# Kernel optimization log

Measured on AMD Instinct MI355X. Metric: run time of the kernel, lower is better.

Reference implementation:

```python
import jax, jax.numpy as jnp
import numpy as np

# RosaAttention config constants
H = 16       # num_rosa_heads
KV = 4       # num_rosa_key_value_heads
QKB = 64     # num_rosa_query_key_bits
VB = 64      # num_rosa_value_bits
HID = 2048   # hidden_size
TAU = 1.0    # temperature buffer


def setup_inputs() -> dict:
    key = jax.random.key(0)
    ks = jax.random.split(key, 8)
    B, S = 2, 2048
    sc = 0.02
    return {
        "x": jax.random.normal(ks[0], (B, S, HID), jnp.float32),
        "attention_mask": jnp.ones((B, S), jnp.int32),
        "Wq": jax.random.normal(ks[1], (HID, H * QKB), jnp.float32) * sc,
        "Wk": jax.random.normal(ks[2], (HID, KV * QKB), jnp.float32) * sc,
        "Wv": jax.random.normal(ks[3], (HID, KV * VB), jnp.float32) * sc,
        "Wo": jax.random.normal(ks[4], (H * VB, HID), jnp.float32) * sc,
        "emb0": jnp.full((H, VB), -1e-05, jnp.float32),
        "emb1": jnp.full((H, VB), +1e-05, jnp.float32),
    }


def reference(x, attention_mask, Wq, Wk, Wv, Wo, emb0, emb1):
    B, S, _ = x.shape
    rep = H // KV
    # projections -> [b, s, heads, bits]
    xq = (x @ Wq).reshape(B, S, H, QKB)
    xk = (x @ Wk).reshape(B, S, KV, QKB)
    xv = (x @ Wv).reshape(B, S, KV, VB)
    # repeat_kv: each kv head repeated n_rep times contiguously
    xk = jnp.repeat(xk, rep, axis=2)   # [b, s, H, QKB]
    xv = jnp.repeat(xv, rep, axis=2)   # [b, s, H, VB]
    # soft bit quantization of q/k, tau-scaled bit-similarity score
    qb = jnp.tanh(xq)
    kb = jnp.tanh(xk)
    scores = jnp.einsum('bqhd,bkhd->bhqk', qb, kb) / (TAU * QKB)
    # causal mask + padding mask (mask True = attend)
    causal = jnp.tril(jnp.ones((S, S), bool))
    mask = causal[None, None] & attention_mask.astype(bool)[:, None, None, :]
    scores = jnp.where(mask, scores, jnp.finfo(scores.dtype).min)
    probs = jax.nn.softmax(scores, axis=-1)        # [b, h, q, k]
    # soft-binarized values: per-bit probabilities, attended, then mapped
    # through learned per-head bit embeddings emb0 (bit=0) / emb1 (bit=1)
    vp = jax.nn.sigmoid(xv)                        # [b, s, H, VB]
    ctx = jnp.einsum('bhqk,bkhv->bqhv', probs, vp) # [b, s, H, VB]
    out_bits = ctx * emb1[None, None] + (1.0 - ctx) * emb0[None, None]
    out = out_bits.reshape(B, S, H * VB) @ Wo      # [b, s, HID]
    return out
```

## Files before the change

kernel.cpp:

```cpp
#include <hip/hip_runtime.h>
#include <math.h>

typedef short bf16x8 __attribute__((ext_vector_type(8)));
typedef float f32x4 __attribute__((ext_vector_type(4)));
typedef float f32x16 __attribute__((ext_vector_type(16)));
typedef unsigned int u32x2 __attribute__((ext_vector_type(2)));
typedef unsigned int u32x4 __attribute__((ext_vector_type(4)));

#define MFMA_BF16(A,B,C) __builtin_amdgcn_mfma_f32_16x16x32_bf16(A,B,C,0,0,0)
#define MFMA32(A,B,C)    __builtin_amdgcn_mfma_f32_32x32x16_bf16(A,B,C,0,0,0)

#define VMCNT(N) asm volatile("s_waitcnt vmcnt(" #N ")" ::: "memory")
#define RBAR() do { asm volatile("" ::: "memory"); __builtin_amdgcn_s_barrier(); \
                    asm volatile("" ::: "memory"); } while (0)
#define PERMSWAP(a, b) asm volatile("v_permlane32_swap_b32 %0, %1" : "+v"(a), "+v"(b))

__device__ __forceinline__ unsigned short f2b(float x) {
    union { float f; unsigned int u; } v; v.f = x;
    unsigned int r = v.u + 0x7FFFu + ((v.u >> 16) & 1u);
    return (unsigned short)(r >> 16);
}

__device__ __forceinline__ unsigned int cvtpk(float lo, float hi) {
    unsigned int r;
    asm("v_cvt_pk_bf16_f32 %0, %1, %2" : "=v"(r) : "v"(lo), "v"(hi));
    return r;
}

__device__ __forceinline__ void gload16(const unsigned short* g, unsigned short* l) {
    __builtin_amdgcn_global_load_lds(
        (const __attribute__((address_space(1))) unsigned int*)(g),
        (__attribute__((address_space(3))) unsigned int*)(l),
        16, 0, 0);
}

__global__ __launch_bounds__(256) void conv_bf16(const float* __restrict__ s,
                                                 unsigned short* __restrict__ d, int n)
{
    int i = blockIdx.x * blockDim.x + threadIdx.x;
    int stride = gridDim.x * blockDim.x;
    for (int idx = i * 4; idx < n; idx += stride * 4) {
        float4 v = *(const float4*)(s + idx);
        ushort4 o;
        o.x = f2b(v.x); o.y = f2b(v.y); o.z = f2b(v.z); o.w = f2b(v.w);
        *(ushort4*)(d + idx) = o;
    }
}

__global__ __launch_bounds__(256) void transp_conv_qkv(const float* __restrict__ Wq,
                                                       const float* __restrict__ Wk,
                                                       const float* __restrict__ Wv,
                                                       unsigned short* __restrict__ dst)
{
    __shared__ float t[32][33];
    const int tx = threadIdx.x, ty = threadIdx.y;
    int bx = blockIdx.x;
    const float* src; int C, cb, dco;
    if (bx < 32)      { src = Wq; C = 1024; cb = bx;      dco = 0; }
    else if (bx < 40) { src = Wk; C = 256;  cb = bx - 32; dco = 1024; }
    else              { src = Wv; C = 256;  cb = bx - 40; dco = 1280; }
    const int c = cb * 32 + tx;
    const int r0 = blockIdx.y * 32;
#pragma unroll
    for (int i = 0; i < 4; ++i)
        t[ty + i * 8][tx] = src[(size_t)(r0 + ty + i * 8) * C + c];
    __syncthreads();
    const int cc = cb * 32 + ty;
#pragma unroll
    for (int i = 0; i < 4; ++i)
        dst[(size_t)(dco + cc + i * 8) * 2048 + r0 + tx] = f2b(t[tx][ty + i * 8]);
}

__global__ __launch_bounds__(256) void transp_conv(const float* __restrict__ src, int R, int C,
                                                   unsigned short* __restrict__ dst, int pitch)
{
    __shared__ float t[32][33];
    const int tx = threadIdx.x, ty = threadIdx.y;
    const int c = blockIdx.x * 32 + tx;
    const int r0 = blockIdx.y * 32;
#pragma unroll
    for (int i = 0; i < 4; ++i)
        t[ty + i * 8][tx] = src[(size_t)(r0 + ty + i * 8) * C + c];
    __syncthreads();
    const int cc = blockIdx.x * 32 + ty;
#pragma unroll
    for (int i = 0; i < 4; ++i)
        dst[(size_t)(cc + i * 8) * pitch + r0 + tx] = f2b(t[tx][ty + i * 8]);
}

__device__ __forceinline__ void stage_g(const unsigned short* AgL, const unsigned short* BgL,
                                        int K, int k0s,
                                        unsigned short* Asb, unsigned short* Bsb, int w)
{
#pragma unroll
    for (int t = 0; t < 4; ++t) {
        const int sub = t >> 1, half = t & 1;
        gload16(AgL + (size_t)(half * 16) * K + k0s + sub * 32,
                Asb + sub * 4096 + (w * 2 + half) * 512);
    }
#pragma unroll
    for (int kk = 0; kk < 2; ++kk)
        gload16(BgL + k0s + kk * 32, Bsb + kk * 2048 + w * 512);
}

template <int MODE>
__global__ __launch_bounds__(256, 3) void gemm_bt_mfma(
    const unsigned short* __restrict__ A,
    const unsigned short* __restrict__ Bt,
    int M, int N, int K,
    float* __restrict__ Cf,
    unsigned short* __restrict__ qh,
    unsigned short* __restrict__ kh,
    unsigned short* __restrict__ vtt)
{
    __shared__ __align__(16) unsigned short As[2][2 * 128 * 32];
    __shared__ __align__(16) unsigned short Bs[2][2 * 64 * 32];

    const int tid = threadIdx.x;
    const int w = tid >> 6, lane = tid & 63, l15 = lane & 15, quad = lane >> 4;
    const int wm = w & 1, wn = w >> 1;
    const int m0 = blockIdx.y * 128, n0 = blockIdx.x * 64;

    const int dsrow = lane >> 2;
    const int dscol = ((lane & 3) ^ ((lane >> 3) & 3)) * 8;
    const int sl8   = (((lane & 15) << 2) | ((lane >> 4) ^ ((lane >> 1) & 3))) * 8;

    f32x4 acc[4][2];
    const f32x4 zero4 = {0.f, 0.f, 0.f, 0.f};
#pragma unroll
    for (int i = 0; i < 4; ++i)
#pragma unroll
        for (int j = 0; j < 2; ++j) acc[i][j] = zero4;

    const unsigned short* AgL = A  + (size_t)(m0 + w * 32 + dsrow) * K + dscol;
    const unsigned short* BgL = Bt + (size_t)(n0 + w * 16 + dsrow) * K + dscol;

    const int NT = K >> 6;
    stage_g(AgL, BgL, K, 0, &As[0][0], &Bs[0][0], w);

    int cb = 0;
    for (int t = 0; t < NT; ++t) {
        if (t + 1 < NT) {
            stage_g(AgL, BgL, K, (t + 1) * 64, &As[cb ^ 1][0], &Bs[cb ^ 1][0], w);
            VMCNT(6);
        } else {
            VMCNT(0);
        }
        RBAR();

        bf16x8 af[4][2], bf[2][2];
#pragma unroll
        for (int kk = 0; kk < 2; ++kk) {
#pragma unroll
            for (int mt = 0; mt < 4; ++mt)
                af[mt][kk] = *(const bf16x8*)&As[cb][kk * 4096 + (wm * 4 + mt) * 512 + sl8];
#pragma unroll
            for (int nt = 0; nt < 2; ++nt)
                bf[nt][kk] = *(const bf16x8*)&Bs[cb][kk * 2048 + (wn * 2 + nt) * 512 + sl8];
        }
#pragma unroll
        for (int kk = 0; kk < 2; ++kk)
#pragma unroll
            for (int mt = 0; mt < 4; ++mt)
#pragma unroll
                for (int nt = 0; nt < 2; ++nt)
                    acc[mt][nt] = MFMA_BF16(af[mt][kk], bf[nt][kk], acc[mt][nt]);

        if (t + 1 < NT) RBAR();
        cb ^= 1;
    }

    if (MODE == 0) {
#pragma unroll
        for (int mt = 0; mt < 4; ++mt)
#pragma unroll
            for (int nt = 0; nt < 2; ++nt) {
                const int gn = n0 + wn * 32 + nt * 16 + l15;
#pragma unroll
                for (int r = 0; r < 4; ++r) {
                    const int gm = m0 + wm * 64 + mt * 16 + quad * 4 + r;
                    Cf[(size_t)gm * N + gn] = acc[mt][nt][r];
                }
            }
    } else {
        if (n0 < 1024) {
#pragma unroll
            for (int mt = 0; mt < 4; ++mt)
#pragma unroll
                for (int nt = 0; nt < 2; ++nt) {
                    const int gn = n0 + wn * 32 + nt * 16 + l15;
#pragma unroll
                    for (int r = 0; r < 4; ++r) {
                        const int gm = m0 + wm * 64 + mt * 16 + quad * 4 + r;
                        qh[(size_t)gm * 1024 + gn] = f2b(tanhf(acc[mt][nt][r]) * 0.0225421100f);
                    }
                }
        } else if (n0 < 1280) {
#pragma unroll
            for (int mt = 0; mt < 4; ++mt)
#pragma unroll
                for (int nt = 0; nt < 2; ++nt) {
                    const int gn = n0 + wn * 32 + nt * 16 + l15 - 1024;
#pragma unroll
                    for (int r = 0; r < 4; ++r) {
                        const int gm = m0 + wm * 64 + mt * 16 + quad * 4 + r;
                        kh[(size_t)gm * 256 + gn] = f2b(tanhf(acc[mt][nt][r]));
                    }
                }
        } else {
#pragma unroll
            for (int mt = 0; mt < 4; ++mt)
#pragma unroll
                for (int nt = 0; nt < 2; ++nt) {
                    const int gn = n0 + wn * 32 + nt * 16 + l15 - 1280;
                    const int g = gn >> 6, vv = gn & 63;
                    const int s0 = m0 + wm * 64 + mt * 16 + quad * 4;
                    const int b = s0 >> 11, sl = s0 & 2047;
                    ushort4 pk;
                    unsigned short* pp = (unsigned short*)&pk;
#pragma unroll
                    for (int r = 0; r < 4; ++r) {
                        float sv = 1.0f / (1.0f + __expf(-acc[mt][nt][r]));
                        pp[r] = f2b(sv);
                    }
                    *(ushort4*)&vtt[((size_t)(b * 4 + g) * 64 + vv) * 2048 + sl] = pk;
                }
        }
    }
}

__global__ __launch_bounds__(256, 4) void rosa_attn_mfma(
    const unsigned short* __restrict__ qh,
    const unsigned short* __restrict__ kh,
    const unsigned short* __restrict__ vtt,
    const int* __restrict__ amask,
    const float* __restrict__ emb0,
    const float* __restrict__ emb1,
    unsigned short* __restrict__ ob)
{
    __shared__ __align__(16) unsigned short Ks[2][4096];
    __shared__ __align__(16) unsigned short Vs[2][4096];
    __shared__ unsigned int Mflg[4];
    __shared__ float Lred[2][2][32];

    const int a = blockIdx.x & 7, m = blockIdx.x >> 3;
    const int h = blockIdx.y, b = blockIdx.z, g = h >> 2;
    const int hb = h + 16 * b;
    const int sel = (m + (hb >> 3)) & 3;
    const int qt = (sel == 0) ? a : (sel == 1) ? 15 - a : (sel == 2) ? 16 + a : 31 - a;

    const int tid = threadIdx.x;
    const int w = tid >> 6, lane = tid & 63;
    const int kq = w >> 1, qq = w & 1;
    const int l31 = lane & 31, H = lane >> 5, x7 = lane & 7;

    const int srow = lane >> 3;
    const int scol = ((lane & 7) ^ srow) * 8;
    const unsigned short* kst0 = kh + ((size_t)(b * 2048) + w * 16 + srow) * 256 + g * 64 + scol;
    const unsigned short* vst0 = vtt + ((size_t)(b * 4 + g) * 64 + w * 16 + srow) * 2048 + scol;
    const int* mbase = amask + b * 2048;

    int kadr[4];
#pragma unroll
    for (int mi = 0; mi < 4; ++mi)
        kadr[mi] = (kq * 32 + l31) * 64 + (((mi * 2 + H) ^ x7) * 8);
    int vadr[2][2];
#pragma unroll
    for (int vh = 0; vh < 2; ++vh)
#pragma unroll
        for (int kc = 0; kc < 2; ++kc)
            vadr[vh][kc] = (vh * 32 + l31) * 64 + (((kq * 4 + kc * 2 + H) ^ x7) * 8);

    unsigned int cbits = 0;
#pragma unroll
    for (int r = 0; r < 16; ++r) {
        const int kl = (r & 3) + 8 * (r >> 2) + 4 * H;
        if (kl <= l31) cbits |= (1u << r);
    }

    const int q0 = qt * 64, nkt = qt + 1;

#define STAGE_TILE(k0s, buf)                                                   \
    {                                                                          \
        gload16(kst0 + (size_t)(k0s) * 256,        &Ks[buf][(w * 16) * 64]);   \
        gload16(kst0 + (size_t)(k0s) * 256 + 2048, &Ks[buf][(w * 16 + 8) * 64]);\
        gload16(vst0 + (k0s),                      &Vs[buf][(w * 16) * 64]);   \
        gload16(vst0 + (k0s) + 16384,              &Vs[buf][(w * 16 + 8) * 64]);\
    }

    const int4 mv0 = *(const int4*)(mbase + tid * 8);
    const int4 mv1 = *(const int4*)(mbase + tid * 8 + 4);

    STAGE_TILE(0, 0)

    const unsigned short* qp = qh + ((size_t)(b * 2048 + q0 + qq * 32 + l31) * 16 + h) * 64 + H * 8;
    const bf16x8 qf0 = *(const bf16x8*)(qp);
    const bf16x8 qf1 = *(const bf16x8*)(qp + 16);
    const bf16x8 qf2 = *(const bf16x8*)(qp + 32);
    const bf16x8 qf3 = *(const bf16x8*)(qp + 48);

    const bool f8 = mv0.x && mv0.y && mv0.z && mv0.w && mv1.x && mv1.y && mv1.z && mv1.w;
    const unsigned long long bal = __ballot(f8);
    const bool bytefull = ((bal >> ((lane & 7) * 8)) & 0xFFull) == 0xFFull;
    const unsigned long long bal2 = __ballot(bytefull && (lane < 8));
    if (lane == 0) Mflg[w] = (unsigned int)(bal2 & 0xFFull);
    RBAR();
    const unsigned int mflags = Mflg[0] | (Mflg[1] << 8) | (Mflg[2] << 16) | (Mflg[3] << 24);

    const f32x16 z16 = {0.f,0.f,0.f,0.f, 0.f,0.f,0.f,0.f, 0.f,0.f,0.f,0.f, 0.f,0.f,0.f,0.f};
    f32x16 oacc0 = z16, oacc1 = z16;
    float psum = 0.0f;
    const bool skipdiag = (kq > qq);

    int cb = 0;
    for (int kt = 0; kt < nkt; ++kt) {
        if (kt + 1 < nkt) {
            STAGE_TILE((kt + 1) * 64, cb ^ 1)
            VMCNT(4);
        } else {
            VMCNT(0);
        }
        RBAR();

        const bool diag = (kt == qt);
        if (!(diag && skipdiag)) {
            const bf16x8 kf0 = *(const bf16x8*)&Ks[cb][kadr[0]];
            const bf16x8 kf1 = *(const bf16x8*)&Ks[cb][kadr[1]];
            const bf16x8 kf2 = *(const bf16x8*)&Ks[cb][kadr[2]];
            const bf16x8 kf3 = *(const bf16x8*)&Ks[cb][kadr[3]];
            __builtin_amdgcn_s_setprio(1);
            f32x16 sc = MFMA32(kf0, qf0, z16);
            sc = MFMA32(kf1, qf1, sc);
            sc = MFMA32(kf2, qf2, sc);
            sc = MFMA32(kf3, qf3, sc);
            __builtin_amdgcn_s_setprio(0);

            float p[16];
#pragma unroll
            for (int r = 0; r < 16; ++r) p[r] = __builtin_exp2f(sc[r]);
            if (diag && kq == qq) {
#pragma unroll
                for (int r = 0; r < 16; ++r)
                    if (!((cbits >> r) & 1u)) p[r] = 0.0f;
            }
            if (!((mflags >> kt) & 1u)) {
#pragma unroll
                for (int r = 0; r < 16; ++r) {
                    const int kgl = kt * 64 + kq * 32 + (r & 3) + 8 * (r >> 2) + 4 * H;
                    if (mbase[kgl] == 0) p[r] = 0.0f;
                }
            }
            psum += (((p[0]+p[1])+(p[2]+p[3])) + ((p[4]+p[5])+(p[6]+p[7])))
                  + (((p[8]+p[9])+(p[10]+p[11])) + ((p[12]+p[13])+(p[14]+p[15])));

            unsigned int W0 = cvtpk(p[0],  p[1]),  W1 = cvtpk(p[2],  p[3]);
            unsigned int W2 = cvtpk(p[4],  p[5]),  W3 = cvtpk(p[6],  p[7]);
            unsigned int W4 = cvtpk(p[8],  p[9]),  W5 = cvtpk(p[10], p[11]);
            unsigned int W6 = cvtpk(p[12], p[13]), W7 = cvtpk(p[14], p[15]);
            PERMSWAP(W0, W2);  PERMSWAP(W1, W3);
            PERMSWAP(W4, W6);  PERMSWAP(W5, W7);
            u32x4 paw0; paw0[0] = W0; paw0[1] = W1; paw0[2] = W2; paw0[3] = W3;
            u32x4 paw1; paw1[0] = W4; paw1[1] = W5; paw1[2] = W6; paw1[3] = W7;
            const bf16x8 pa0 = __builtin_bit_cast(bf16x8, paw0);
            const bf16x8 pa1 = __builtin_bit_cast(bf16x8, paw1);

            const bf16x8 vb00 = *(const bf16x8*)&Vs[cb][vadr[0][0]];
            const bf16x8 vb01 = *(const bf16x8*)&Vs[cb][vadr[0][1]];
            const bf16x8 vb10 = *(const bf16x8*)&Vs[cb][vadr[1][0]];
            const bf16x8 vb11 = *(const bf16x8*)&Vs[cb][vadr[1][1]];
            __builtin_amdgcn_s_setprio(1);
            oacc0 = MFMA32(pa0, vb00, oacc0);
            oacc0 = MFMA32(pa1, vb01, oacc0);
            oacc1 = MFMA32(pa0, vb10, oacc1);
            oacc1 = MFMA32(pa1, vb11, oacc1);
            __builtin_amdgcn_s_setprio(0);
        }

        if (kt + 1 < nkt) { RBAR(); cb ^= 1; }
    }

    psum += __shfl_xor(psum, 32);

    RBAR();

    if (H == 0) Lred[kq][qq][l31] = psum;

    float* Ored = (float*)&Ks[0][0];
    const int slw = qq * 2 + (1 - kq);
    if (kq == 0) {
#pragma unroll
        for (int c = 0; c < 4; ++c) {
            float4 t = {oacc1[c*4+0], oacc1[c*4+1], oacc1[c*4+2], oacc1[c*4+3]};
            *(float4*)&Ored[slw * 1024 + lane * 16 + ((c ^ (lane & 3)) * 4)] = t;
        }
    } else {
#pragma unroll
        for (int c = 0; c < 4; ++c) {
            float4 t = {oacc0[c*4+0], oacc0[c*4+1], oacc0[c*4+2], oacc0[c*4+3]};
            *(float4*)&Ored[slw * 1024 + lane * 16 + ((c ^ (lane & 3)) * 4)] = t;
        }
    }
    RBAR();

    const int slr = qq * 2 + kq;
    f32x16 osum = (kq == 0) ? oacc0 : oacc1;
#pragma unroll
    for (int c = 0; c < 4; ++c) {
        float4 t = *(const float4*)&Ored[slr * 1024 + lane * 16 + ((c ^ (lane & 3)) * 4)];
        osum[c*4+0] += t.x; osum[c*4+1] += t.y; osum[c*4+2] += t.z; osum[c*4+3] += t.w;
    }

    float rl[16];
#pragma unroll
    for (int r = 0; r < 16; ++r) {
        const int ql = (r & 3) + 8 * (r >> 2) + 4 * H;
        rl[r] = __builtin_amdgcn_rcpf(Lred[0][qq][ql] + Lred[1][qq][ql]);
    }

    const int vg = kq * 32 + l31;
    const float e0 = emb0[h * 64 + vg];
    const float ed = emb1[h * 64 + vg] - e0;
    unsigned short* obp = ob + ((size_t)(b * 2048 + q0 + qq * 32) * 16 + h) * 64 + vg;
#pragma unroll
    for (int r = 0; r < 16; ++r) {
        const int ql = (r & 3) + 8 * (r >> 2) + 4 * H;
        const float val = e0 + (osum[r] * rl[r]) * ed;
        obp[(size_t)ql * 1024] = f2b(val);
    }
#undef STAGE_TILE
}

extern "C" void kernel_launch(void* const* d_in, const int* in_sizes, int n_in,
                              void* d_out, int out_size, void* d_ws, size_t ws_size,
                              hipStream_t stream)
{
    const float* x    = (const float*)d_in[0];
    const int*   amask= (const int*)d_in[1];
    const float* Wq   = (const float*)d_in[2];
    const float* Wk   = (const float*)d_in[3];
    const float* Wv   = (const float*)d_in[4];
    const float* Wo   = (const float*)d_in[5];
    const float* emb0 = (const float*)d_in[6];
    const float* emb1 = (const float*)d_in[7];
    float* out = (float*)d_out;

    char* base = (char*)d_ws;
    unsigned short* xh    = (unsigned short*)(base);
    unsigned short* ob    = xh;
    unsigned short* Wqkvt = (unsigned short*)(base + (16u << 20));
    unsigned short* Wot   = (unsigned short*)(base + (22u << 20));
    unsigned short* qh    = (unsigned short*)(base + (26u << 20));
    unsigned short* kh    = (unsigned short*)(base + (34u << 20));
    unsigned short* vtt   = (unsigned short*)(base + (36u << 20));

    conv_bf16<<<2048, 256, 0, stream>>>(x, xh, 4096 * 2048);
    transp_conv_qkv<<<dim3(48, 64), dim3(32, 8), 0, stream>>>(Wq, Wk, Wv, Wqkvt);
    transp_conv<<<dim3(64, 32), dim3(32, 8), 0, stream>>>(Wo, 1024, 2048, Wot, 1024);

    gemm_bt_mfma<1><<<dim3(24, 32), 256, 0, stream>>>(xh, Wqkvt, 4096, 1536, 2048,
                                                      nullptr, qh, kh, vtt);
    rosa_attn_mfma<<<dim3(32, 16, 2), 256, 0, stream>>>(qh, kh, vtt, amask, emb0, emb1, ob);
    gemm_bt_mfma<0><<<dim3(32, 32), 256, 0, stream>>>(ob, Wot, 4096, 2048, 1024,
                                                      out, nullptr, nullptr, nullptr);
}
```

Before: 223.6 us.

## Fuse prep kernels, remap GEMM block order, enlarge output GEMM tile, reswizzle LDS

Merges the three conversion/transpose kernels into one prep launch to remove launch overhead and tail gaps. Splits the templated GEMM into a dedicated QKV kernel and an output-projection kernel. The output GEMM now uses 128x128 tiles with a larger LDS footprint and occupancy 2. Both GEMMs get a blockIdx remap that groups tiles for L2 locality. The attention reduction scratch gets a different XOR swizzle meant to cut LDS bank conflicts.

```diff
diff --git a/kernel.cpp b/kernel.cpp
--- a/kernel.cpp
+++ b/kernel.cpp
@@ -34,63 +34,69 @@
         16, 0, 0);
 }
 
-__global__ __launch_bounds__(256) void conv_bf16(const float* __restrict__ s,
-                                                 unsigned short* __restrict__ d, int n)
-{
-    int i = blockIdx.x * blockDim.x + threadIdx.x;
-    int stride = gridDim.x * blockDim.x;
-    for (int idx = i * 4; idx < n; idx += stride * 4) {
-        float4 v = *(const float4*)(s + idx);
-        ushort4 o;
-        o.x = f2b(v.x); o.y = f2b(v.y); o.z = f2b(v.z); o.w = f2b(v.w);
-        *(ushort4*)(d + idx) = o;
-    }
-}
-
-__global__ __launch_bounds__(256) void transp_conv_qkv(const float* __restrict__ Wq,
-                                                       const float* __restrict__ Wk,
-                                                       const float* __restrict__ Wv,
-                                                       unsigned short* __restrict__ dst)
+__global__ __launch_bounds__(256) void prep(
+    const float* __restrict__ x, unsigned short* __restrict__ xh,
+    const float* __restrict__ Wq, const float* __restrict__ Wk,
+    const float* __restrict__ Wv, unsigned short* __restrict__ Wqkvt,
+    const float* __restrict__ Wo, unsigned short* __restrict__ Wot)
 {
     __shared__ float t[32][33];
-    const int tx = threadIdx.x, ty = threadIdx.y;
-    int bx = blockIdx.x;
-    const float* src; int C, cb, dco;
-    if (bx < 32)      { src = Wq; C = 1024; cb = bx;      dco = 0; }
-    else if (bx < 40) { src = Wk; C = 256;  cb = bx - 32; dco = 1024; }
-    else              { src = Wv; C = 256;  cb = bx - 40; dco = 1280; }
-    const int c = cb * 32 + tx;
-    const int r0 = blockIdx.y * 32;
-#pragma unroll
-    for (int i = 0; i < 4; ++i)
-        t[ty + i * 8][tx] = src[(size_t)(r0 + ty + i * 8) * C + c];
-    __syncthreads();
-    const int cc = cb * 32 + ty;
-#pragma unroll
-    for (int i = 0; i < 4; ++i)
-        dst[(size_t)(dco + cc + i * 8) * 2048 + r0 + tx] = f2b(t[tx][ty + i * 8]);
-}
-
-__global__ __launch_bounds__(256) void transp_conv(const float* __restrict__ src, int R, int C,
-                                                   unsigned short* __restrict__ dst, int pitch)
-{
-    __shared__ float t[32][33];
-    const int tx = threadIdx.x, ty = threadIdx.y;
-    const int c = blockIdx.x * 32 + tx;
-    const int r0 = blockIdx.y * 32;
-#pragma unroll
-    for (int i = 0; i < 4; ++i)
-        t[ty + i * 8][tx] = src[(size_t)(r0 + ty + i * 8) * C + c];
-    __syncthreads();
-    const int cc = blockIdx.x * 32 + ty;
-#pragma unroll
-    for (int i = 0; i < 4; ++i)
-        dst[(size_t)(cc + i * 8) * pitch + r0 + tx] = f2b(t[tx][ty + i * 8]);
-}
-
-__device__ __forceinline__ void stage_g(const unsigned short* AgL, const unsigned short* BgL,
-                                        int K, int k0s,
-                                        unsigned short* Asb, unsigned short* Bsb, int w)
+    const int bid = blockIdx.x, tid = threadIdx.x;
+
+    if (bid < 2048) {
+        const int n = 4096 * 2048;
+        int i = bid * 256 + tid;
+        int stride = 2048 * 256;
+        for (int idx = i * 4; idx < n; idx += stride * 4) {
+            float4 v = *(const float4*)(x + idx);
+            ushort4 o;
+            o.x = f2b(v.x); o.y = f2b(v.y); o.z = f2b(v.z); o.w = f2b(v.w);
+            *(ushort4*)(xh + idx) = o;
+        }
+        return;
+    }
+
+    const int tx = tid & 31, ty = tid >> 5;
+
+    if (bid < 5120) {
+        const int idx = bid - 2048;
+        const int bx = idx % 48, by = idx / 48;
+        const float* src; int C, cb, dco;
+        if (bx < 32)      { src = Wq; C = 1024; cb = bx;      dco = 0; }
+        else if (bx < 40) { src = Wk; C = 256;  cb = bx - 32; dco = 1024; }
+        else              { src = Wv; C = 256;  cb = bx - 40; dco = 1280; }
+        const int c = cb * 32 + tx;
+        const int r0 = by * 32;
+#pragma unroll
+        for (int i = 0; i < 4; ++i)
+            t[ty + i * 8][tx] = src[(size_t)(r0 + ty + i * 8) * C + c];
+        __syncthreads();
+        const int cc = cb * 32 + ty;
+#pragma unroll
+        for (int i = 0; i < 4; ++i)
+            Wqkvt[(size_t)(dco + cc + i * 8) * 2048 + r0 + tx] = f2b(t[tx][ty + i * 8]);
+        return;
+    }
+
+    {
+        const int idx = bid - 5120;
+        const int bx = idx % 64, by = idx / 64;
+        const int c = bx * 32 + tx;
+        const int r0 = by * 32;
+#pragma unroll
+        for (int i = 0; i < 4; ++i)
+            t[ty + i * 8][tx] = Wo[(size_t)(r0 + ty + i * 8) * 2048 + c];
+        __syncthreads();
+        const int cc = bx * 32 + ty;
+#pragma unroll
+        for (int i = 0; i < 4; ++i)
+            Wot[(size_t)(cc + i * 8) * 1024 + r0 + tx] = f2b(t[tx][ty + i * 8]);
+    }
+}
+
+__device__ __forceinline__ void stage_qkv(const unsigned short* AgL, const unsigned short* BgL,
+                                          int K, int k0s,
+                                          unsigned short* Asb, unsigned short* Bsb, int w)
 {
 #pragma unroll
     for (int t = 0; t < 4; ++t) {
@@ -103,12 +109,9 @@
         gload16(BgL + k0s + kk * 32, Bsb + kk * 2048 + w * 512);
 }
 
-template <int MODE>
-__global__ __launch_bounds__(256, 3) void gemm_bt_mfma(
+__global__ __launch_bounds__(256, 3) void gemm_qkv(
     const unsigned short* __restrict__ A,
     const unsigned short* __restrict__ Bt,
-    int M, int N, int K,
-    float* __restrict__ Cf,
     unsigned short* __restrict__ qh,
     unsigned short* __restrict__ kh,
     unsigned short* __restrict__ vtt)
@@ -116,10 +119,14 @@
     __shared__ __align__(16) unsigned short As[2][2 * 128 * 32];
     __shared__ __align__(16) unsigned short Bs[2][2 * 64 * 32];
 
+    const int K = 2048;
     const int tid = threadIdx.x;
     const int w = tid >> 6, lane = tid & 63, l15 = lane & 15, quad = lane >> 4;
     const int wm = w & 1, wn = w >> 1;
-    const int m0 = blockIdx.y * 128, n0 = blockIdx.x * 64;
+
+    const int orig = blockIdx.x + 24 * blockIdx.y;
+    const int lb = (orig & 7) * 96 + (orig >> 3);
+    const int m0 = (lb / 24) * 128, n0 = (lb % 24) * 64;
 
     const int dsrow = lane >> 2;
     const int dscol = ((lane & 3) ^ ((lane >> 3) & 3)) * 8;
@@ -136,12 +143,12 @@
     const unsigned short* BgL = Bt + (size_t)(n0 + w * 16 + dsrow) * K + dscol;
 
     const int NT = K >> 6;
-    stage_g(AgL, BgL, K, 0, &As[0][0], &Bs[0][0], w);
+    stage_qkv(AgL, BgL, K, 0, &As[0][0], &Bs[0][0], w);
 
     int cb = 0;
     for (int t = 0; t < NT; ++t) {
         if (t + 1 < NT) {
-            stage_g(AgL, BgL, K, (t + 1) * 64, &As[cb ^ 1][0], &Bs[cb ^ 1][0], w);
+            stage_qkv(AgL, BgL, K, (t + 1) * 64, &As[cb ^ 1][0], &Bs[cb ^ 1][0], w);
             VMCNT(6);
         } else {
             VMCNT(0);
@@ -170,7 +177,7 @@
         cb ^= 1;
     }
 
-    if (MODE == 0) {
+    if (n0 < 1024) {
 #pragma unroll
         for (int mt = 0; mt < 4; ++mt)
 #pragma unroll
@@ -179,54 +186,131 @@
 #pragma unroll
                 for (int r = 0; r < 4; ++r) {
                     const int gm = m0 + wm * 64 + mt * 16 + quad * 4 + r;
-                    Cf[(size_t)gm * N + gn] = acc[mt][nt][r];
+                    qh[(size_t)gm * 1024 + gn] = f2b(tanhf(acc[mt][nt][r]) * 0.0225421100f);
+                }
+            }
+    } else if (n0 < 1280) {
+#pragma unroll
+        for (int mt = 0; mt < 4; ++mt)
+#pragma unroll
+            for (int nt = 0; nt < 2; ++nt) {
+                const int gn = n0 + wn * 32 + nt * 16 + l15 - 1024;
+#pragma unroll
+                for (int r = 0; r < 4; ++r) {
+                    const int gm = m0 + wm * 64 + mt * 16 + quad * 4 + r;
+                    kh[(size_t)gm * 256 + gn] = f2b(tanhf(acc[mt][nt][r]));
                 }
             }
     } else {
-        if (n0 < 1024) {
+#pragma unroll
+        for (int mt = 0; mt < 4; ++mt)
+#pragma unroll
+            for (int nt = 0; nt < 2; ++nt) {
+                const int gn = n0 + wn * 32 + nt * 16 + l15 - 1280;
+                const int g = gn >> 6, vv = gn & 63;
+                const int s0 = m0 + wm * 64 + mt * 16 + quad * 4;
+                const int b = s0 >> 11, sl = s0 & 2047;
+                ushort4 pk;
+                unsigned short* pp = (unsigned short*)&pk;
+#pragma unroll
+                for (int r = 0; r < 4; ++r) {
+                    float sv = 1.0f / (1.0f + __expf(-acc[mt][nt][r]));
+                    pp[r] = f2b(sv);
+                }
+                *(ushort4*)&vtt[((size_t)(b * 4 + g) * 64 + vv) * 2048 + sl] = pk;
+            }
+    }
+}
+
+__device__ __forceinline__ void stage_out(const unsigned short* AgL, const unsigned short* BgL,
+                                          int K, int k0s,
+                                          unsigned short* Asb, unsigned short* Bsb, int w)
+{
+#pragma unroll
+    for (int t = 0; t < 4; ++t) {
+        const int sub = t >> 1, half = t & 1;
+        gload16(AgL + (size_t)(half * 16) * K + k0s + sub * 32,
+                Asb + sub * 4096 + (w * 2 + half) * 512);
+        gload16(BgL + (size_t)(half * 16) * K + k0s + sub * 32,
+                Bsb + sub * 4096 + (w * 2 + half) * 512);
+    }
+}
+
+__global__ __launch_bounds__(256, 2) void gemm_out(
+    const unsigned short* __restrict__ A,
+    const unsigned short* __restrict__ Bt,
+    float* __restrict__ Cf)
+{
+    __shared__ __align__(16) unsigned short As[2][8192];
+    __shared__ __align__(16) unsigned short Bs[2][8192];
+
+    const int K = 1024, N = 2048;
+    const int tid = threadIdx.x;
+    const int w = tid >> 6, lane = tid & 63, l15 = lane & 15, quad = lane >> 4;
+    const int wm = w & 1, wn = w >> 1;
+
+    const int orig = blockIdx.x + 16 * blockIdx.y;
+    const int lb = (orig & 7) * 64 + (orig >> 3);
+    const int m0 = (lb >> 4) * 128, n0 = (lb & 15) * 128;
+
+    const int dsrow = lane >> 2;
+    const int dscol = ((lane & 3) ^ ((lane >> 3) & 3)) * 8;
+    const int sl8   = (((lane & 15) << 2) | ((lane >> 4) ^ ((lane >> 1) & 3))) * 8;
+
+    f32x4 acc[4][4];
+    const f32x4 zero4 = {0.f, 0.f, 0.f, 0.f};
+#pragma unroll
+    for (int i = 0; i < 4; ++i)
+#pragma unroll
+        for (int j = 0; j < 4; ++j) acc[i][j] = zero4;
+
+    const unsigned short* AgL = A  + (size_t)(m0 + w * 32 + dsrow) * K + dscol;
+    const unsigned short* BgL = Bt + (size_t)(n0 + w * 32 + dsrow) * K + dscol;
+
+    const int NT = K >> 6;
+    stage_out(AgL, BgL, K, 0, &As[0][0], &Bs[0][0], w);
+
+    int cb = 0;
+    for (int t = 0; t < NT; ++t) {
+        if (t + 1 < NT) {
+            stage_out(AgL, BgL, K, (t + 1) * 64, &As[cb ^ 1][0], &Bs[cb ^ 1][0], w);
+            VMCNT(8);
+        } else {
+            VMCNT(0);
+        }
+        RBAR();
+
+#pragma unroll
+        for (int kk = 0; kk < 2; ++kk) {
+            bf16x8 af[4], bf[4];
 #pragma unroll
             for (int mt = 0; mt < 4; ++mt)
-#pragma unroll
-                for (int nt = 0; nt < 2; ++nt) {
-                    const int gn = n0 + wn * 32 + nt * 16 + l15;
-#pragma unroll
-                    for (int r = 0; r < 4; ++r) {
-                        const int gm = m0 + wm * 64 + mt * 16 + quad * 4 + r;
-                        qh[(size_t)gm * 1024 + gn] = f2b(tanhf(acc[mt][nt][r]) * 0.0225421100f);
-                    }
-                }
-        } else if (n0 < 1280) {
+                af[mt] = *(const bf16x8*)&As[cb][kk * 4096 + (wm * 4 + mt) * 512 + sl8];
+#pragma unroll
+            for (int nt = 0; nt < 4; ++nt)
+                bf[nt] = *(const bf16x8*)&Bs[cb][kk * 4096 + (wn * 4 + nt) * 512 + sl8];
 #pragma unroll
             for (int mt = 0; mt < 4; ++mt)
 #pragma unroll
-                for (int nt = 0; nt < 2; ++nt) {
-                    const int gn = n0 + wn * 32 + nt * 16 + l15 - 1024;
-#pragma unroll
-                    for (int r = 0; r < 4; ++r) {
-                        const int gm = m0 + wm * 64 + mt * 16 + quad * 4 + r;
-                        kh[(size_t)gm * 256 + gn] = f2b(tanhf(acc[mt][nt][r]));
-                    }
-                }
-        } else {
-#pragma unroll
-            for (int mt = 0; mt < 4; ++mt)
-#pragma unroll
-                for (int nt = 0; nt < 2; ++nt) {
-                    const int gn = n0 + wn * 32 + nt * 16 + l15 - 1280;
-                    const int g = gn >> 6, vv = gn & 63;
-                    const int s0 = m0 + wm * 64 + mt * 16 + quad * 4;
-                    const int b = s0 >> 11, sl = s0 & 2047;
-                    ushort4 pk;
-                    unsigned short* pp = (unsigned short*)&pk;
-#pragma unroll
-                    for (int r = 0; r < 4; ++r) {
-                        float sv = 1.0f / (1.0f + __expf(-acc[mt][nt][r]));
-                        pp[r] = f2b(sv);
-                    }
-                    *(ushort4*)&vtt[((size_t)(b * 4 + g) * 64 + vv) * 2048 + sl] = pk;
-                }
-        }
-    }
+                for (int nt = 0; nt < 4; ++nt)
+                    acc[mt][nt] = MFMA_BF16(af[mt], bf[nt], acc[mt][nt]);
+        }
+
+        if (t + 1 < NT) RBAR();
+        cb ^= 1;
+    }
+
+#pragma unroll
+    for (int mt = 0; mt < 4; ++mt)
+#pragma unroll
+        for (int nt = 0; nt < 4; ++nt) {
+            const int gn = n0 + wn * 64 + nt * 16 + l15;
+#pragma unroll
+            for (int r = 0; r < 4; ++r) {
+                const int gm = m0 + wm * 64 + mt * 16 + quad * 4 + r;
+                Cf[(size_t)gm * N + gn] = acc[mt][nt][r];
+            }
+        }
 }
 
 __global__ __launch_bounds__(256, 4) void rosa_attn_mfma(
@@ -387,17 +471,18 @@
 
     float* Ored = (float*)&Ks[0][0];
     const int slw = qq * 2 + (1 - kq);
+    const int cx = (lane & 3) ^ ((lane >> 2) & 3);
     if (kq == 0) {
 #pragma unroll
         for (int c = 0; c < 4; ++c) {
             float4 t = {oacc1[c*4+0], oacc1[c*4+1], oacc1[c*4+2], oacc1[c*4+3]};
-            *(float4*)&Ored[slw * 1024 + lane * 16 + ((c ^ (lane & 3)) * 4)] = t;
+            *(float4*)&Ored[slw * 1024 + lane * 16 + ((c ^ cx) * 4)] = t;
         }
     } else {
 #pragma unroll
         for (int c = 0; c < 4; ++c) {
             float4 t = {oacc0[c*4+0], oacc0[c*4+1], oacc0[c*4+2], oacc0[c*4+3]};
-            *(float4*)&Ored[slw * 1024 + lane * 16 + ((c ^ (lane & 3)) * 4)] = t;
+            *(float4*)&Ored[slw * 1024 + lane * 16 + ((c ^ cx) * 4)] = t;
         }
     }
     RBAR();
@@ -406,7 +491,7 @@
     f32x16 osum = (kq == 0) ? oacc0 : oacc1;
 #pragma unroll
     for (int c = 0; c < 4; ++c) {
-        float4 t = *(const float4*)&Ored[slr * 1024 + lane * 16 + ((c ^ (lane & 3)) * 4)];
+        float4 t = *(const float4*)&Ored[slr * 1024 + lane * 16 + ((c ^ cx) * 4)];
         osum[c*4+0] += t.x; osum[c*4+1] += t.y; osum[c*4+2] += t.z; osum[c*4+3] += t.w;
     }
 
@@ -453,13 +538,9 @@
     unsigned short* kh    = (unsigned short*)(base + (34u << 20));
     unsigned short* vtt   = (unsigned short*)(base + (36u << 20));
 
-    conv_bf16<<<2048, 256, 0, stream>>>(x, xh, 4096 * 2048);
-    transp_conv_qkv<<<dim3(48, 64), dim3(32, 8), 0, stream>>>(Wq, Wk, Wv, Wqkvt);
-    transp_conv<<<dim3(64, 32), dim3(32, 8), 0, stream>>>(Wo, 1024, 2048, Wot, 1024);
-
-    gemm_bt_mfma<1><<<dim3(24, 32), 256, 0, stream>>>(xh, Wqkvt, 4096, 1536, 2048,
-                                                      nullptr, qh, kh, vtt);
+    prep<<<7168, 256, 0, stream>>>(x, xh, Wq, Wk, Wv, Wqkvt, Wo, Wot);
+
+    gemm_qkv<<<dim3(24, 32), 256, 0, stream>>>(xh, Wqkvt, qh, kh, vtt);
     rosa_attn_mfma<<<dim3(32, 16, 2), 256, 0, stream>>>(qh, kh, vtt, amask, emb0, emb1, ob);
-    gemm_bt_mfma<0><<<dim3(32, 32), 256, 0, stream>>>(ob, Wot, 4096, 2048, 1024,
-                                                      out, nullptr, nullptr, nullptr);
-}
+    gemm_out<<<dim3(16, 32), 256, 0, stream>>>(ob, Wot, out);
+}
```

Measured after the change: 213.9 us. 4.3% less time.
